# Kernel tuning notes

Hardware: AMD Instinct MI355X
Metric: run time of the kernel (lower is better)

The kernel has to match this reference:

```python
import jax, jax.numpy as jnp
import numpy as np

VOCAB = 81616
EMB = 32
B = 16384
NNZ = 200


def setup_inputs() -> dict:
    key = jax.random.key(0)
    k1, k2 = jax.random.split(key)
    indices = jax.random.randint(k1, (B, NNZ), 0, VOCAB, dtype=jnp.int32)
    values = jnp.ones((B, NNZ), dtype=jnp.float32)  # multi-hot sparse values
    w = jax.random.normal(k2, (VOCAB, EMB), dtype=jnp.float32) * 0.05
    b = jnp.zeros((EMB,), dtype=jnp.float32)
    return {"indices": indices, "values": values, "w": w, "b": b}


def reference(indices, values, w, b):
    # Equivalent to tf.matmul(tf.sparse.to_dense(inputs), w) + b, but computed
    # by gathering only the nonzero rows of the score matrix.
    # w[indices]: [B, NNZ, EMB]; weighted sum over NNZ -> [B, EMB]
    gathered = w[indices]
    out = jnp.einsum('bn,bne->be', values, gathered) + b
    return out
```

## Files before the change

kernel.cpp:

```cpp
#include <hip/hip_runtime.h>


constexpr int NNZ = 200;
constexpr int ROWS_PER_BLOCK = 32;
constexpr int THREADS = 256;

__global__ __launch_bounds__(THREADS) void playlist_embedding_kernel(
    const int* __restrict__ indices,
    const float* __restrict__ values,
    const float* __restrict__ w,
    const float* __restrict__ bias,
    float* __restrict__ out)
{
    __shared__ int   s_idx[ROWS_PER_BLOCK * NNZ];
    __shared__ float s_val[ROWS_PER_BLOCK * NNZ];

    const int tid = threadIdx.x;
    const int block_row0 = blockIdx.x * ROWS_PER_BLOCK;

    const int total = ROWS_PER_BLOCK * NNZ;
    const int* __restrict__ g_idx = indices + (size_t)block_row0 * NNZ;
    const float* __restrict__ g_val = values + (size_t)block_row0 * NNZ;
    #pragma unroll
    for (int i = tid; i < total; i += THREADS) {
        s_idx[i] = g_idx[i];
        s_val[i] = g_val[i];
    }
    __syncthreads();

    const int c = tid & 7;
    const int r = tid >> 3;

    const float4* __restrict__ w4 = (const float4*)w;
    const float4 bias4 = ((const float4*)bias)[c];

    const int*   __restrict__ row_idx = s_idx + r * NNZ;
    const float* __restrict__ row_val = s_val + r * NNZ;

    float ax = 0.f, ay = 0.f, az = 0.f, aw = 0.f;
    #pragma unroll 8
    for (int n = 0; n < NNZ; ++n) {
        const int u = row_idx[n];
        const float v = row_val[n];
        const float4 wv = w4[u * 8 + c];
        ax += v * wv.x;
        ay += v * wv.y;
        az += v * wv.z;
        aw += v * wv.w;
    }

    float4 o;
    o.x = ax + bias4.x;
    o.y = ay + bias4.y;
    o.z = az + bias4.z;
    o.w = aw + bias4.w;
    ((float4*)out)[(size_t)(block_row0 + r) * 8 + c] = o;
}

extern "C" void kernel_launch(void* const* d_in, const int* in_sizes, int n_in,
                              void* d_out, int out_size, void* d_ws, size_t ws_size,
                              hipStream_t stream) {
    const int*   indices = (const int*)d_in[0];
    const float* values  = (const float*)d_in[1];
    const float* w       = (const float*)d_in[2];
    const float* bias    = (const float*)d_in[3];
    float* out = (float*)d_out;

    const int B = in_sizes[0] / NNZ;
    const int grid = B / ROWS_PER_BLOCK;

    playlist_embedding_kernel<<<grid, THREADS, 0, stream>>>(
        indices, values, w, bias, out);
}
```

Before: 44.01 us.

## Assign one row per wavefront and split NNZ across lanes with shuffle reduction

The old shared-memory staging of indices and values and its block barrier are removed. Each 64-lane wavefront now handles one batch row: 8 lane groups take interleaved NNZ slots, each lane loads a float4 slice of the gathered embedding, and the partial sums are combined with xor shuffles. This gives many more blocks with no LDS, which should raise occupancy and memory-level parallelism for the random gathers. In exchange it adds shuffle-reduction work and per-lane global loads of the index and value arrays.

```diff
diff --git a/kernel.cpp b/kernel.cpp
--- a/kernel.cpp
+++ b/kernel.cpp
@@ -2,59 +2,58 @@
 
 
 constexpr int NNZ = 200;
-constexpr int ROWS_PER_BLOCK = 32;
 constexpr int THREADS = 256;
 
-__global__ __launch_bounds__(THREADS) void playlist_embedding_kernel(
+__global__ __launch_bounds__(THREADS, 6) void playlist_embedding_kernel(
     const int* __restrict__ indices,
     const float* __restrict__ values,
     const float* __restrict__ w,
     const float* __restrict__ bias,
     float* __restrict__ out)
 {
-    __shared__ int   s_idx[ROWS_PER_BLOCK * NNZ];
-    __shared__ float s_val[ROWS_PER_BLOCK * NNZ];
+    const int tid    = threadIdx.x;
+    const int wave   = tid >> 6;
+    const int lane   = tid & 63;
+    const int n_slot = lane >> 3;
+    const int c      = lane & 7;
 
-    const int tid = threadIdx.x;
-    const int block_row0 = blockIdx.x * ROWS_PER_BLOCK;
+    const int row = blockIdx.x * 4 + wave;
 
-    const int total = ROWS_PER_BLOCK * NNZ;
-    const int* __restrict__ g_idx = indices + (size_t)block_row0 * NNZ;
-    const float* __restrict__ g_val = values + (size_t)block_row0 * NNZ;
-    #pragma unroll
-    for (int i = tid; i < total; i += THREADS) {
-        s_idx[i] = g_idx[i];
-        s_val[i] = g_val[i];
-    }
-    __syncthreads();
-
-    const int c = tid & 7;
-    const int r = tid >> 3;
-
+    const int*   __restrict__ ri = indices + (size_t)row * NNZ;
+    const float* __restrict__ rv = values  + (size_t)row * NNZ;
     const float4* __restrict__ w4 = (const float4*)w;
-    const float4 bias4 = ((const float4*)bias)[c];
-
-    const int*   __restrict__ row_idx = s_idx + r * NNZ;
-    const float* __restrict__ row_val = s_val + r * NNZ;
 
     float ax = 0.f, ay = 0.f, az = 0.f, aw = 0.f;
-    #pragma unroll 8
-    for (int n = 0; n < NNZ; ++n) {
-        const int u = row_idx[n];
-        const float v = row_val[n];
-        const float4 wv = w4[u * 8 + c];
+
+    #pragma unroll 5
+    for (int k = 0; k < NNZ / 8; ++k) {
+        const int n = n_slot + (k << 3);
+        const int   u = ri[n];
+        const float v = rv[n];
+        const float4 wv = w4[(size_t)u * 8 + c];
         ax += v * wv.x;
         ay += v * wv.y;
         az += v * wv.z;
         aw += v * wv.w;
     }
 
-    float4 o;
-    o.x = ax + bias4.x;
-    o.y = ay + bias4.y;
-    o.z = az + bias4.z;
-    o.w = aw + bias4.w;
-    ((float4*)out)[(size_t)(block_row0 + r) * 8 + c] = o;
+    #pragma unroll
+    for (int mask = 8; mask <= 32; mask <<= 1) {
+        ax += __shfl_xor(ax, mask);
+        ay += __shfl_xor(ay, mask);
+        az += __shfl_xor(az, mask);
+        aw += __shfl_xor(aw, mask);
+    }
+
+    if (n_slot == 0) {
+        const float4 bias4 = ((const float4*)bias)[c];
+        float4 o;
+        o.x = ax + bias4.x;
+        o.y = ay + bias4.y;
+        o.z = az + bias4.z;
+        o.w = aw + bias4.w;
+        ((float4*)out)[(size_t)row * 8 + c] = o;
+    }
 }
 
 extern "C" void kernel_launch(void* const* d_in, const int* in_sizes, int n_in,
@@ -67,7 +66,7 @@
     float* out = (float*)d_out;
 
     const int B = in_sizes[0] / NNZ;
-    const int grid = B / ROWS_PER_BLOCK;
+    const int grid = B / 4;
 
     playlist_embedding_kernel<<<grid, THREADS, 0, stream>>>(
         indices, values, w, bias, out);
```

New measurement: 46.85 us. 1.06x slower.
